# Optimization experiments

Measured on AMD Instinct MI355X. Metric: run time of the kernel, lower is better.

## Reference

```python
import jax, jax.numpy as jnp
import numpy as np

EMB_DIM = 2048
HIDDEN_DIM = 8192
BATCH = 4
SEQ = 2048


def _kaiming_normal(key, out_f, in_f):
    # kaiming_normal_(mode='fan_in', nonlinearity='relu'): std = sqrt(2 / fan_in)
    std = np.sqrt(2.0 / in_f).astype(np.float32)
    return jax.random.normal(key, (out_f, in_f), dtype=jnp.float32) * std


def setup_inputs() -> dict:
    key = jax.random.key(0)
    kx, k1, k2, k3 = jax.random.split(key, 4)
    x = jax.random.normal(kx, (BATCH, SEQ, EMB_DIM), dtype=jnp.float32)
    w1 = _kaiming_normal(k1, HIDDEN_DIM, EMB_DIM)   # fc1.weight [hidden, emb]
    w2 = _kaiming_normal(k2, HIDDEN_DIM, EMB_DIM)   # fc2.weight [hidden, emb]
    w3 = _kaiming_normal(k3, EMB_DIM, HIDDEN_DIM)   # fc3.weight [emb, hidden]
    return {"x": x, "w1": w1, "w2": w2, "w3": w3, "scale_x": 1}


def reference(x, w1, w2, w3, scale_x):
    # fc1/fc2: x @ W.T  (no bias). scale_x is unused in the fp (calibration) path.
    gate = jnp.einsum('bse,he->bsh', x, w1)  # [B,S,H]
    up = jnp.einsum('bse,he->bsh', x, w2)    # [B,S,H]
    h = jax.nn.silu(gate) * up               # Custom_SiLU + Custom_ElementWiseMul
    out = jnp.einsum('bsh,eh->bse', h, w3)   # fc3 down-projection
    return out
```

## Files before the change

kernel.cpp:

```cpp
#include <hip/hip_runtime.h>
#include <hip/hip_bf16.h>

#define M_ROWS 8192
#define E_DIM  2048
#define H_DIM  8192

typedef __attribute__((ext_vector_type(8))) short bf16x8;
typedef __attribute__((ext_vector_type(4))) float f32x4;
typedef __attribute__((ext_vector_type(4))) unsigned int uint4v;

__device__ __forceinline__ unsigned short f2bf_rne(float x) {
  unsigned u = __builtin_bit_cast(unsigned, x);
  u += 0x7FFFu + ((u >> 16) & 1u);
  return (unsigned short)(u >> 16);
}

__global__ __launch_bounds__(256) void cvt4_f32_bf16(const float* __restrict__ s0, unsigned short* __restrict__ d0,
                                                     const float* __restrict__ s1, unsigned short* __restrict__ d1,
                                                     const float* __restrict__ s2, unsigned short* __restrict__ d2,
                                                     const float* __restrict__ s3, unsigned short* __restrict__ d3,
                                                     int n8) {
  int i = blockIdx.x * blockDim.x + threadIdx.x;
  if (i >= n8) return;
  const float* in = (blockIdx.y == 0) ? s0 : (blockIdx.y == 1) ? s1 : (blockIdx.y == 2) ? s2 : s3;
  unsigned short* out = (blockIdx.y == 0) ? d0 : (blockIdx.y == 1) ? d1 : (blockIdx.y == 2) ? d2 : d3;
  const float4* p = (const float4*)(in + (size_t)i * 8);
  float4 a = p[0];
  float4 b = p[1];
  union { unsigned short us[8]; uint4v v; } r;
  r.us[0] = f2bf_rne(a.x); r.us[1] = f2bf_rne(a.y);
  r.us[2] = f2bf_rne(a.z); r.us[3] = f2bf_rne(a.w);
  r.us[4] = f2bf_rne(b.x); r.us[5] = f2bf_rne(b.y);
  r.us[6] = f2bf_rne(b.z); r.us[7] = f2bf_rne(b.w);
  *(uint4v*)(out + (size_t)i * 8) = r.v;
}

__device__ __forceinline__ void gld_lds16(const unsigned short* g, unsigned short* l) {
  __builtin_amdgcn_global_load_lds(
      (const __attribute__((address_space(1))) unsigned int*)g,
      (__attribute__((address_space(3))) unsigned int*)l, 16, 0, 0);
}

#define VMCNT(n)   asm volatile("s_waitcnt vmcnt(" #n ")" ::: "memory")

template <int EPI>
__global__ __launch_bounds__(512, 2)
void gemm256(const unsigned short* __restrict__ A,
             const unsigned short* __restrict__ B,
             const unsigned short* __restrict__ B2,
             void* __restrict__ Cout,
             int M, int N, int K) {
  __shared__ unsigned short sh[65536];
  unsigned short* lAb = sh;
  unsigned short* lBb = sh + 32768;

  const int tid = threadIdx.x;
  const int lane = tid & 63;
  const int wave = tid >> 6;
  const int wr = wave >> 2;
  const int wc = wave & 3;
  const int wrow = wave >> 1;
  const int wcol = wave & 1;
  const int lr = lane & 15, lk = lane >> 4;

  const int gx = gridDim.x;
  const int wg = blockIdx.y * gx + blockIdx.x;
  int bcol, brow;
  if constexpr (EPI == 3) {
    const int xcd = wg & 7, idx = wg >> 3;
    bcol = xcd * 8 + (idx & 7);
    brow = idx >> 3;
  } else {
    const int nwg = gx * gridDim.y;
    const int swz = (wg & 7) * (nwg >> 3) + (wg >> 3);
    bcol = swz % gx;
    brow = swz / gx;
  }

  const unsigned short* Ag = A + (size_t)brow * 256 * K;
  const unsigned short* BgH0;
  const unsigned short* BgH1;
  if constexpr (EPI == 3) {
    BgH0 = B  + (size_t)bcol * 128 * K;
    BgH1 = B2 + (size_t)bcol * 128 * K;
  } else {
    BgH0 = B + (size_t)bcol * 256 * K;
    BgH1 = BgH0 + (size_t)128 * K;
  }

  f32x4 acc[8][4] = {};
  const int NT = K >> 6;
  const int NI = NT >> 1;

  auto stageH = [&](const unsigned short* gbase, unsigned short* ldsh) {
#pragma unroll
    for (int i = 0; i < 2; ++i) {
      int p = i * 4096 + tid * 8;
      int row = p >> 6;
      int lslot = ((p >> 3) & 7) ^ (row & 7);
      gld_lds16(gbase + (size_t)row * K + lslot * 8, ldsh + p);
    }
  };

  const int xsw = (lr & 7) << 3;
  bf16x8 af[8][2], bf[4][2], bu[4][2];

#define RD_PH1(LA, LB) \
  if constexpr (EPI == 3) { \
    _Pragma("unroll") for (int m = 0; m < 4; ++m) { \
      int r = wrow * 64 + m * 16 + lr; \
      af[m][0] = *(const bf16x8*)&LA[(r * 64 + lk * 8) ^ xsw]; \
      af[m][1] = *(const bf16x8*)&LA[(r * 64 + 32 + lk * 8) ^ xsw]; } \
    _Pragma("unroll") for (int n = 0; n < 2; ++n) { \
      int r = wcol * 64 + n * 16 + lr; \
      bf[n][0] = *(const bf16x8*)&LB[(r * 64 + lk * 8) ^ xsw]; \
      bf[n][1] = *(const bf16x8*)&LB[(r * 64 + 32 + lk * 8) ^ xsw]; } \
  } else { \
    _Pragma("unroll") for (int m = 0; m < 4; ++m) { \
      int r = wr * 128 + m * 16 + lr; \
      af[m][0] = *(const bf16x8*)&LA[(r * 64 + lk * 8) ^ xsw]; \
      af[m][1] = *(const bf16x8*)&LA[(r * 64 + 32 + lk * 8) ^ xsw]; } \
    _Pragma("unroll") for (int n = 0; n < 2; ++n) { \
      int r = wc * 64 + n * 16 + lr; \
      bf[n][0] = *(const bf16x8*)&LB[(r * 64 + lk * 8) ^ xsw]; \
      bf[n][1] = *(const bf16x8*)&LB[(r * 64 + 32 + lk * 8) ^ xsw]; } \
  }
#define RD_PH2(LB) \
  { \
    const int wcx = (EPI == 3) ? wcol : wc; \
    _Pragma("unroll") for (int n = 2; n < 4; ++n) { \
      int r = wcx * 64 + n * 16 + lr; \
      bf[n][0] = *(const bf16x8*)&LB[(r * 64 + lk * 8) ^ xsw]; \
      bf[n][1] = *(const bf16x8*)&LB[(r * 64 + 32 + lk * 8) ^ xsw]; } \
  }
#define RD_PH3(LA, LB) \
  if constexpr (EPI == 3) { \
    _Pragma("unroll") for (int n = 0; n < 4; ++n) { \
      int r = wcol * 64 + n * 16 + lr; \
      bu[n][0] = *(const bf16x8*)&LB[8192 + ((r * 64 + lk * 8) ^ xsw)]; \
      bu[n][1] = *(const bf16x8*)&LB[8192 + ((r * 64 + 32 + lk * 8) ^ xsw)]; } \
  } else { \
    _Pragma("unroll") for (int m = 4; m < 8; ++m) { \
      int r = wr * 128 + m * 16 + lr; \
      af[m][0] = *(const bf16x8*)&LA[(r * 64 + lk * 8) ^ xsw]; \
      af[m][1] = *(const bf16x8*)&LA[(r * 64 + 32 + lk * 8) ^ xsw]; } \
  }
#define PH_CORE_BEGIN \
  __builtin_amdgcn_s_barrier(); \
  asm volatile("s_waitcnt lgkmcnt(0)" ::: "memory"); \
  __builtin_amdgcn_sched_barrier(0); \
  __builtin_amdgcn_s_setprio(1);
#define PH_CORE_END __builtin_amdgcn_s_setprio(0);
#define MF(ACC_M, AV, BV) \
  acc[ACC_M][n] = __builtin_amdgcn_mfma_f32_16x16x32_bf16(AV[ks], BV[ks], acc[ACC_M][n], 0, 0, 0);
#define PH_MFMA_Q(Q) \
  PH_CORE_BEGIN \
  if constexpr (EPI == 3) { \
    if constexpr (Q == 1) { _Pragma("unroll") for (int m = 0; m < 4; ++m) _Pragma("unroll") for (int n = 0; n < 2; ++n) _Pragma("unroll") for (int ks = 0; ks < 2; ++ks) MF(m, af[m], bf[n]) } \
    if constexpr (Q == 2) { _Pragma("unroll") for (int m = 0; m < 4; ++m) _Pragma("unroll") for (int n = 2; n < 4; ++n) _Pragma("unroll") for (int ks = 0; ks < 2; ++ks) MF(m, af[m], bf[n]) } \
    if constexpr (Q == 3) { _Pragma("unroll") for (int m = 0; m < 4; ++m) _Pragma("unroll") for (int n = 0; n < 2; ++n) _Pragma("unroll") for (int ks = 0; ks < 2; ++ks) MF(m + 4, af[m], bu[n]) } \
    if constexpr (Q == 4) { _Pragma("unroll") for (int m = 0; m < 4; ++m) _Pragma("unroll") for (int n = 2; n < 4; ++n) _Pragma("unroll") for (int ks = 0; ks < 2; ++ks) MF(m + 4, af[m], bu[n]) } \
  } else { \
    if constexpr (Q == 1) { _Pragma("unroll") for (int m = 0; m < 4; ++m) _Pragma("unroll") for (int n = 0; n < 2; ++n) _Pragma("unroll") for (int ks = 0; ks < 2; ++ks) MF(m, af[m], bf[n]) } \
    if constexpr (Q == 2) { _Pragma("unroll") for (int m = 0; m < 4; ++m) _Pragma("unroll") for (int n = 2; n < 4; ++n) _Pragma("unroll") for (int ks = 0; ks < 2; ++ks) MF(m, af[m], bf[n]) } \
    if constexpr (Q == 3) { _Pragma("unroll") for (int m = 4; m < 8; ++m) _Pragma("unroll") for (int n = 0; n < 2; ++n) _Pragma("unroll") for (int ks = 0; ks < 2; ++ks) MF(m, af[m], bf[n]) } \
    if constexpr (Q == 4) { _Pragma("unroll") for (int m = 4; m < 8; ++m) _Pragma("unroll") for (int n = 2; n < 4; ++n) _Pragma("unroll") for (int ks = 0; ks < 2; ++ks) MF(m, af[m], bf[n]) } \
  } \
  PH_CORE_END

  stageH(Ag, lAb);
  stageH(Ag + (size_t)128 * K, lAb + 8192);
  stageH(BgH0, lBb);
  stageH(BgH1, lBb + 8192);
  stageH(Ag + 64, lAb + 16384);
  stageH(Ag + (size_t)128 * K + 64, lAb + 16384 + 8192);
  stageH(BgH0 + 64, lBb + 16384);
  stageH(BgH1 + 64, lBb + 16384 + 8192);
  VMCNT(0);
  __builtin_amdgcn_s_barrier();

  const unsigned short* lA0 = lAb;
  const unsigned short* lB0 = lBb;
  const unsigned short* lA1 = lAb + 16384;
  const unsigned short* lB1 = lBb + 16384;

  for (int it = 0; it < NI; ++it) {
    const int t = it << 1;
    const size_t kT1 = (size_t)(t + 1) * 64;
    const size_t kS2 = (size_t)((t + 2 < NT) ? t + 2 : NT - 1) * 64;
    const size_t kS3 = (size_t)((t + 3 < NT) ? t + 3 : NT - 1) * 64;

    RD_PH1(lA0, lB0);
    if (it > 0) stageH(Ag + (size_t)128 * K + kT1, lAb + 16384 + 8192);
    asm volatile("s_waitcnt lgkmcnt(8)" ::: "memory");
    PH_MFMA_Q(1);
    __builtin_amdgcn_s_barrier();

    RD_PH2(lB0);
    PH_MFMA_Q(2);
    __builtin_amdgcn_s_barrier();

    RD_PH3(lA0, lB0);
    stageH(BgH0 + kS2, lBb);
    PH_MFMA_Q(3);
    __builtin_amdgcn_s_barrier();

    stageH(BgH1 + kS2, lBb + 8192);
    stageH(Ag + kS2, lAb);
    PH_MFMA_Q(4);
    VMCNT(6);
    __builtin_amdgcn_s_barrier();

    RD_PH1(lA1, lB1);
    stageH(Ag + (size_t)128 * K + kS2, lAb + 8192);
    asm volatile("s_waitcnt lgkmcnt(8)" ::: "memory");
    PH_MFMA_Q(1);
    __builtin_amdgcn_s_barrier();

    RD_PH2(lB1);
    PH_MFMA_Q(2);
    __builtin_amdgcn_s_barrier();

    RD_PH3(lA1, lB1);
    stageH(BgH0 + kS3, lBb + 16384);
    PH_MFMA_Q(3);
    __builtin_amdgcn_s_barrier();

    stageH(BgH1 + kS3, lBb + 16384 + 8192);
    stageH(Ag + kS3, lAb + 16384);
    PH_MFMA_Q(4);
    VMCNT(6);
    __builtin_amdgcn_s_barrier();
  }
  VMCNT(0);

#undef RD_PH1
#undef RD_PH2
#undef RD_PH3
#undef PH_CORE_BEGIN
#undef PH_CORE_END
#undef MF
#undef PH_MFMA_Q

  if constexpr (EPI == 3) {
    const int row0 = brow * 256 + wrow * 64 + lk * 4;
    const int col0 = bcol * 128 + wcol * 64 + lr;
#pragma unroll
    for (int m = 0; m < 4; ++m)
#pragma unroll
      for (int n = 0; n < 4; ++n)
#pragma unroll
        for (int j = 0; j < 4; ++j) {
          float g = acc[m][n][j];
          float u = acc[m + 4][n][j];
          float s = g / (1.0f + __expf(-g));
          ((unsigned short*)Cout)[(size_t)(row0 + m * 16 + j) * N + (col0 + n * 16)] =
              f2bf_rne(s * u);
        }
  } else {
    const int row0 = brow * 256 + wr * 128 + lk * 4;
    const int col0 = bcol * 256 + wc * 64 + lr;
#pragma unroll
    for (int m = 0; m < 8; ++m)
#pragma unroll
      for (int n = 0; n < 4; ++n)
#pragma unroll
        for (int j = 0; j < 4; ++j) {
          size_t idx = (size_t)(row0 + m * 16 + j) * N + (col0 + n * 16);
          ((float*)Cout)[idx] = acc[m][n][j];
        }
  }
}

extern "C" void kernel_launch(void* const* d_in, const int* in_sizes, int n_in,
                              void* d_out, int out_size, void* d_ws, size_t ws_size,
                              hipStream_t stream) {
  const float* x  = (const float*)d_in[0];
  const float* w1 = (const float*)d_in[1];
  const float* w2 = (const float*)d_in[2];
  const float* w3 = (const float*)d_in[3];
  float* out = (float*)d_out;

  const int M = M_ROWS, E = E_DIM, H = H_DIM;

  unsigned short* xb  = (unsigned short*)d_ws;
  unsigned short* w1b = xb + (size_t)M * E;
  unsigned short* w2b = w1b + (size_t)H * E;
  unsigned short* hb  = w2b + (size_t)H * E;

  const int n8 = (M * E) / 8;
  const size_t need_hoist = ((size_t)M * E + 2 * (size_t)H * E + (size_t)M * H + (size_t)E * H) * 2;

  if (ws_size >= need_hoist) {
    unsigned short* w3b = hb + (size_t)M * H;
    cvt4_f32_bf16<<<dim3(n8 / 256, 4), 256, 0, stream>>>(x, xb, w1, w1b, w2, w2b, w3, w3b, n8);
    gemm256<3><<<dim3(H / 128, M / 256), 512, 0, stream>>>(xb, w1b, w2b, hb, M, H, E);
    gemm256<0><<<dim3(E / 256, M / 256), 512, 0, stream>>>(hb, w3b, nullptr, out, M, E, H);
  } else {
    unsigned short* w3b = xb;
    cvt4_f32_bf16<<<dim3(n8 / 256, 3), 256, 0, stream>>>(x, xb, w1, w1b, w2, w2b, nullptr, nullptr, n8);
    gemm256<3><<<dim3(H / 128, M / 256), 512, 0, stream>>>(xb, w1b, w2b, hb, M, H, E);
    cvt4_f32_bf16<<<dim3(n8 / 256, 1), 256, 0, stream>>>(w3, w3b, nullptr, nullptr, nullptr, nullptr, nullptr, nullptr, n8);
    gemm256<0><<<dim3(E / 256, M / 256), 512, 0, stream>>>(hb, w3b, nullptr, out, M, E, H);
  }
}
```

Measured before the change: 776.4 us.

## Process two row tiles per workgroup in gate/up GEMM with cross-tile prefetch

The fused gate/up GEMM now launches 1024 workgroups, each computing two consecutive 256-row tiles for one column block. Loads for the next tile's first K-steps are issued during the tail of the current tile, so the pipeline does not drain and refill between tiles, and the same B panel stays hot in cache. The SiLU epilogue runs after each sub-tile and the accumulators are then reset. This halves the grid, which shortens the tail of partial waves but gives each workgroup a longer serial run and leaves fewer workgroups to balance across CUs.

```diff
diff --git a/kernel.cpp b/kernel.cpp
--- a/kernel.cpp
+++ b/kernel.cpp
@@ -65,19 +65,19 @@
 
   const int gx = gridDim.x;
   const int wg = blockIdx.y * gx + blockIdx.x;
-  int bcol, brow;
+  const int NSUB = (EPI == 3) ? 2 : 1;
+  int bcol, brow0;
   if constexpr (EPI == 3) {
     const int xcd = wg & 7, idx = wg >> 3;
     bcol = xcd * 8 + (idx & 7);
-    brow = idx >> 3;
+    brow0 = (idx >> 3) * 2;
   } else {
     const int nwg = gx * gridDim.y;
     const int swz = (wg & 7) * (nwg >> 3) + (wg >> 3);
     bcol = swz % gx;
-    brow = swz / gx;
-  }
-
-  const unsigned short* Ag = A + (size_t)brow * 256 * K;
+    brow0 = swz / gx;
+  }
+
   const unsigned short* BgH0;
   const unsigned short* BgH1;
   if constexpr (EPI == 3) {
@@ -91,6 +91,7 @@
   f32x4 acc[8][4] = {};
   const int NT = K >> 6;
   const int NI = NT >> 1;
+  const int NTm = NT - 1;
 
   auto stageH = [&](const unsigned short* gbase, unsigned short* ldsh) {
 #pragma unroll
@@ -168,15 +169,18 @@
   } \
   PH_CORE_END
 
-  stageH(Ag, lAb);
-  stageH(Ag + (size_t)128 * K, lAb + 8192);
-  stageH(BgH0, lBb);
-  stageH(BgH1, lBb + 8192);
-  stageH(Ag + 64, lAb + 16384);
-  stageH(Ag + (size_t)128 * K + 64, lAb + 16384 + 8192);
-  stageH(BgH0 + 64, lBb + 16384);
-  stageH(BgH1 + 64, lBb + 16384 + 8192);
-  VMCNT(0);
+  {
+    const unsigned short* Ag0  = A + (size_t)brow0 * 256 * K;
+    const unsigned short* Ag0H = Ag0 + (size_t)128 * K;
+    stageH(Ag0, lAb);
+    stageH(Ag0H, lAb + 8192);
+    stageH(BgH0, lBb);
+    stageH(BgH1, lBb + 8192);
+    stageH(Ag0 + 64, lAb + 16384);
+    stageH(BgH0 + 64, lBb + 16384);
+    stageH(BgH1 + 64, lBb + 16384 + 8192);
+  }
+  VMCNT(6);
   __builtin_amdgcn_s_barrier();
 
   const unsigned short* lA0 = lAb;
@@ -184,53 +188,103 @@
   const unsigned short* lA1 = lAb + 16384;
   const unsigned short* lB1 = lBb + 16384;
 
-  for (int it = 0; it < NI; ++it) {
-    const int t = it << 1;
-    const size_t kT1 = (size_t)(t + 1) * 64;
-    const size_t kS2 = (size_t)((t + 2 < NT) ? t + 2 : NT - 1) * 64;
-    const size_t kS3 = (size_t)((t + 3 < NT) ? t + 3 : NT - 1) * 64;
-
-    RD_PH1(lA0, lB0);
-    if (it > 0) stageH(Ag + (size_t)128 * K + kT1, lAb + 16384 + 8192);
-    asm volatile("s_waitcnt lgkmcnt(8)" ::: "memory");
-    PH_MFMA_Q(1);
-    __builtin_amdgcn_s_barrier();
-
-    RD_PH2(lB0);
-    PH_MFMA_Q(2);
-    __builtin_amdgcn_s_barrier();
-
-    RD_PH3(lA0, lB0);
-    stageH(BgH0 + kS2, lBb);
-    PH_MFMA_Q(3);
-    __builtin_amdgcn_s_barrier();
-
-    stageH(BgH1 + kS2, lBb + 8192);
-    stageH(Ag + kS2, lAb);
-    PH_MFMA_Q(4);
-    VMCNT(6);
-    __builtin_amdgcn_s_barrier();
-
-    RD_PH1(lA1, lB1);
-    stageH(Ag + (size_t)128 * K + kS2, lAb + 8192);
-    asm volatile("s_waitcnt lgkmcnt(8)" ::: "memory");
-    PH_MFMA_Q(1);
-    __builtin_amdgcn_s_barrier();
-
-    RD_PH2(lB1);
-    PH_MFMA_Q(2);
-    __builtin_amdgcn_s_barrier();
-
-    RD_PH3(lA1, lB1);
-    stageH(BgH0 + kS3, lBb + 16384);
-    PH_MFMA_Q(3);
-    __builtin_amdgcn_s_barrier();
-
-    stageH(BgH1 + kS3, lBb + 16384 + 8192);
-    stageH(Ag + kS3, lAb + 16384);
-    PH_MFMA_Q(4);
-    VMCNT(6);
-    __builtin_amdgcn_s_barrier();
+  for (int sub = 0; sub < NSUB; ++sub) {
+    const int brow = brow0 + sub;
+    const unsigned short* Ag   = A + (size_t)brow * 256 * K;
+    const unsigned short* AgH1 = Ag + (size_t)128 * K;
+    const int nbrow = (sub + 1 < NSUB) ? brow + 1 : brow;
+    const unsigned short* AgN   = A + (size_t)nbrow * 256 * K;
+    const unsigned short* AgNH1 = AgN + (size_t)128 * K;
+
+    for (int it = 0; it < NI; ++it) {
+      const int t = it << 1;
+      const size_t kT1 = (size_t)(t + 1) * 64;
+      const bool o2 = (t + 2 >= NT);
+      const bool o3 = (t + 3 >= NT);
+      const size_t k2 = (size_t)((t + 2) & NTm) * 64;
+      const size_t k3 = (size_t)((t + 3) & NTm) * 64;
+      const unsigned short* A0s2 = (o2 ? AgN : Ag) + k2;
+      const unsigned short* A1s2 = (o2 ? AgNH1 : AgH1) + k2;
+      const unsigned short* A0s3 = (o3 ? AgN : Ag) + k3;
+
+      RD_PH1(lA0, lB0);
+      stageH(AgH1 + kT1, lAb + 16384 + 8192);
+      asm volatile("s_waitcnt lgkmcnt(8)" ::: "memory");
+      PH_MFMA_Q(1);
+      __builtin_amdgcn_s_barrier();
+
+      RD_PH2(lB0);
+      PH_MFMA_Q(2);
+      __builtin_amdgcn_s_barrier();
+
+      RD_PH3(lA0, lB0);
+      stageH(BgH0 + k2, lBb);
+      PH_MFMA_Q(3);
+      __builtin_amdgcn_s_barrier();
+
+      stageH(BgH1 + k2, lBb + 8192);
+      stageH(A0s2, lAb);
+      PH_MFMA_Q(4);
+      VMCNT(6);
+      __builtin_amdgcn_s_barrier();
+
+      RD_PH1(lA1, lB1);
+      stageH(A1s2, lAb + 8192);
+      asm volatile("s_waitcnt lgkmcnt(8)" ::: "memory");
+      PH_MFMA_Q(1);
+      __builtin_amdgcn_s_barrier();
+
+      RD_PH2(lB1);
+      PH_MFMA_Q(2);
+      __builtin_amdgcn_s_barrier();
+
+      RD_PH3(lA1, lB1);
+      stageH(BgH0 + k3, lBb + 16384);
+      PH_MFMA_Q(3);
+      __builtin_amdgcn_s_barrier();
+
+      stageH(BgH1 + k3, lBb + 16384 + 8192);
+      stageH(A0s3, lAb + 16384);
+      PH_MFMA_Q(4);
+      VMCNT(6);
+      __builtin_amdgcn_s_barrier();
+    }
+
+    if constexpr (EPI == 3) {
+      const int row0 = brow * 256 + wrow * 64 + lk * 4;
+      const int col0 = bcol * 128 + wcol * 64 + lr;
+#pragma unroll
+      for (int m = 0; m < 4; ++m)
+#pragma unroll
+        for (int n = 0; n < 4; ++n)
+#pragma unroll
+          for (int j = 0; j < 4; ++j) {
+            float g = acc[m][n][j];
+            float u = acc[m + 4][n][j];
+            float s = g / (1.0f + __expf(-g));
+            ((unsigned short*)Cout)[(size_t)(row0 + m * 16 + j) * N + (col0 + n * 16)] =
+                f2bf_rne(s * u);
+          }
+      if (sub + 1 < NSUB) {
+#pragma unroll
+        for (int m = 0; m < 8; ++m)
+#pragma unroll
+          for (int n = 0; n < 4; ++n)
+            acc[m][n] = f32x4{0.f, 0.f, 0.f, 0.f};
+      }
+    } else {
+      const int row0 = brow * 256 + wr * 128 + lk * 4;
+      const int col0 = bcol * 256 + wc * 64 + lr;
+#pragma unroll
+      for (int m = 0; m < 8; ++m)
+#pragma unroll
+        for (int n = 0; n < 4; ++n)
+#pragma unroll
+          for (int j = 0; j < 4; ++j) {
+            size_t idx = (size_t)(row0 + m * 16 + j) * N + (col0 + n * 16);
+            ((float*)Cout)[idx] = acc[m][n][j];
+          }
+    }
   }
   VMCNT(0);
 
@@ -241,35 +295,6 @@
 #undef PH_CORE_END
 #undef MF
 #undef PH_MFMA_Q
-
-  if constexpr (EPI == 3) {
-    const int row0 = brow * 256 + wrow * 64 + lk * 4;
-    const int col0 = bcol * 128 + wcol * 64 + lr;
-#pragma unroll
-    for (int m = 0; m < 4; ++m)
-#pragma unroll
-      for (int n = 0; n < 4; ++n)
-#pragma unroll
-        for (int j = 0; j < 4; ++j) {
-          float g = acc[m][n][j];
-          float u = acc[m + 4][n][j];
-          float s = g / (1.0f + __expf(-g));
-          ((unsigned short*)Cout)[(size_t)(row0 + m * 16 + j) * N + (col0 + n * 16)] =
-              f2bf_rne(s * u);
-        }
-  } else {
-    const int row0 = brow * 256 + wr * 128 + lk * 4;
-    const int col0 = bcol * 256 + wc * 64 + lr;
-#pragma unroll
-    for (int m = 0; m < 8; ++m)
-#pragma unroll
-      for (int n = 0; n < 4; ++n)
-#pragma unroll
-        for (int j = 0; j < 4; ++j) {
-          size_t idx = (size_t)(row0 + m * 16 + j) * N + (col0 + n * 16);
-          ((float*)Cout)[idx] = acc[m][n][j];
-        }
-  }
 }
 
 extern "C" void kernel_launch(void* const* d_in, const int* in_sizes, int n_in,
@@ -294,12 +319,12 @@
   if (ws_size >= need_hoist) {
     unsigned short* w3b = hb + (size_t)M * H;
     cvt4_f32_bf16<<<dim3(n8 / 256, 4), 256, 0, stream>>>(x, xb, w1, w1b, w2, w2b, w3, w3b, n8);
-    gemm256<3><<<dim3(H / 128, M / 256), 512, 0, stream>>>(xb, w1b, w2b, hb, M, H, E);
+    gemm256<3><<<dim3(1024), 512, 0, stream>>>(xb, w1b, w2b, hb, M, H, E);
     gemm256<0><<<dim3(E / 256, M / 256), 512, 0, stream>>>(hb, w3b, nullptr, out, M, E, H);
   } else {
     unsigned short* w3b = xb;
     cvt4_f32_bf16<<<dim3(n8 / 256, 3), 256, 0, stream>>>(x, xb, w1, w1b, w2, w2b, nullptr, nullptr, n8);
-    gemm256<3><<<dim3(H / 128, M / 256), 512, 0, stream>>>(xb, w1b, w2b, hb, M, H, E);
+    gemm256<3><<<dim3(1024), 512, 0, stream>>>(xb, w1b, w2b, hb, M, H, E);
     cvt4_f32_bf16<<<dim3(n8 / 256, 1), 256, 0, stream>>>(w3, w3b, nullptr, nullptr, nullptr, nullptr, nullptr, nullptr, n8);
     gemm256<0><<<dim3(E / 256, M / 256), 512, 0, stream>>>(hb, w3b, nullptr, out, M, E, H);
   }
```

New measurement: 754.4 us. 1.03x faster.
